# Performance work log

Measured on AMD Instinct MI355X. Metric: run time of the kernel, lower is better.

## Reference

```python
import jax, jax.numpy as jnp
import numpy as np

D_MODEL = 1024
N_HEADS = 16
HEAD_DIM = D_MODEL // N_HEADS


def setup_inputs() -> dict:
    key = jax.random.key(0)
    kx, kq, kk, kv, ko = jax.random.split(key, 5)
    B, S = 4, 2048
    scale = 0.02
    return {
        "x": jax.random.normal(kx, (B, S, D_MODEL), dtype=jnp.float32),
        "Wq": jax.random.normal(kq, (D_MODEL, D_MODEL), dtype=jnp.float32) * scale,
        "Wk": jax.random.normal(kk, (D_MODEL, HEAD_DIM), dtype=jnp.float32) * scale,
        "Wv": jax.random.normal(kv, (D_MODEL, HEAD_DIM), dtype=jnp.float32) * scale,
        "Wo": jax.random.normal(ko, (D_MODEL, D_MODEL), dtype=jnp.float32) * scale,
    }


def reference(x, Wq, Wk, Wv, Wo):
    B, S, _ = x.shape
    # Q: [B, H, S, hd]; K, V: [B, S, hd] shared across heads (MQA)
    Q = (x @ Wq).reshape(B, S, N_HEADS, HEAD_DIM).transpose(0, 2, 1, 3)
    K = x @ Wk
    V = x @ Wv
    # scores: [B, H, S, S]
    scores = jnp.einsum("bhqd,bkd->bhqk", Q, K) / jnp.sqrt(jnp.float32(HEAD_DIM))
    attn = jax.nn.softmax(scores, axis=-1)
    out = jnp.einsum("bhqk,bkd->bhqd", attn, V)  # [B, H, S, hd]
    out = out.transpose(0, 2, 1, 3).reshape(B, S, D_MODEL)
    return out @ Wo
```

## Files before the change

kernel.cpp:

```cpp
#include <hip/hip_runtime.h>
#include <hip/hip_bf16.h>

typedef __bf16  bf16x8  __attribute__((ext_vector_type(8)));
typedef __bf16  bf16x4  __attribute__((ext_vector_type(4)));
typedef float   f32x4   __attribute__((ext_vector_type(4)));
typedef unsigned short ushort8 __attribute__((ext_vector_type(8)));

#define D_MODEL 1024
#define HEAD_DIM 64
#define N_HEADS 16
#define BATCH 4
#define SEQ 2048
#define ROWS (BATCH*SEQ)
#define QKV_LD 1152
#define VT_LD 2080

#define AS1 __attribute__((address_space(1)))
#define AS3 __attribute__((address_space(3)))

__global__ __launch_bounds__(256) void k_f32_to_bf16(const float* __restrict__ in,
                                                     __bf16* __restrict__ out, int n) {
  int i = (blockIdx.x * 256 + threadIdx.x) * 8;
  if (i >= n) return;
  float4 a = *(const float4*)(in + i);
  float4 b = *(const float4*)(in + i + 4);
  __bf16 r[8] __attribute__((aligned(16))) =
      {(__bf16)a.x,(__bf16)a.y,(__bf16)a.z,(__bf16)a.w,
       (__bf16)b.x,(__bf16)b.y,(__bf16)b.z,(__bf16)b.w};
  *(ushort8*)(out + i) = *(const ushort8*)r;
}

__global__ __launch_bounds__(256) void k_transpose_f32_bf16(const float* __restrict__ in,
                                                            __bf16* __restrict__ out,
                                                            int R, int C) {
  __shared__ float t[32][33];
  int tx = threadIdx.x & 31, ty = threadIdx.x >> 5;
  int r0 = blockIdx.y * 32, c0 = blockIdx.x * 32;
  #pragma unroll
  for (int i = 0; i < 4; ++i)
    t[ty + i*8][tx] = in[(size_t)(r0 + ty + i*8) * C + c0 + tx];
  __syncthreads();
  #pragma unroll
  for (int i = 0; i < 4; ++i)
    out[(size_t)(c0 + ty + i*8) * R + r0 + tx] = (__bf16)t[tx][ty + i*8];
}

template<typename OUT_T>
__global__ __launch_bounds__(256) void k_gemm(const __bf16* __restrict__ A,
                                              const __bf16* __restrict__ Bt,
                                              OUT_T* __restrict__ C,
                                              int M, int N, int K) {
  __shared__ __bf16 As[128*32] __attribute__((aligned(16)));
  __shared__ __bf16 Bs[128*32] __attribute__((aligned(16)));
  const int tid  = threadIdx.x;
  const int lane = tid & 63, wave = tid >> 6;
  const int wm = wave >> 1, wn = wave & 1;
  const int l15 = lane & 15, lhi = lane >> 4;
  const int arow0 = blockIdx.x * 128;
  const int brow0 = blockIdx.y * 128;
  f32x4 acc[4][4] = {};
  const int srow = lane >> 2;
  const int scol = (lane & 3) * 8;

  for (int kt = 0; kt < K; kt += 32) {
    __syncthreads();
    #pragma unroll
    for (int i = 0; i < 2; ++i) {
      int chunk = i*4 + wave;
      int r = chunk*16 + srow;
      __builtin_amdgcn_global_load_lds(
          (const AS1 unsigned int*)(A  + (size_t)(arow0 + r)*K + kt + scol),
          (AS3 unsigned int*)(As + chunk*512), 16, 0, 0);
      __builtin_amdgcn_global_load_lds(
          (const AS1 unsigned int*)(Bt + (size_t)(brow0 + r)*K + kt + scol),
          (AS3 unsigned int*)(Bs + chunk*512), 16, 0, 0);
    }
    __syncthreads();
    bf16x8 af[4], bfr[4];
    #pragma unroll
    for (int m = 0; m < 4; ++m)
      af[m] = *(const bf16x8*)(As + (wm*64 + m*16 + l15)*32 + lhi*8);
    #pragma unroll
    for (int n = 0; n < 4; ++n)
      bfr[n] = *(const bf16x8*)(Bs + (wn*64 + n*16 + l15)*32 + lhi*8);
    #pragma unroll
    for (int m = 0; m < 4; ++m)
      #pragma unroll
      for (int n = 0; n < 4; ++n)
        acc[m][n] = __builtin_amdgcn_mfma_f32_16x16x32_bf16(af[m], bfr[n], acc[m][n], 0, 0, 0);
  }
  #pragma unroll
  for (int m = 0; m < 4; ++m)
    #pragma unroll
    for (int n = 0; n < 4; ++n) {
      int row = arow0 + wm*64 + m*16 + lhi*4;
      int col = brow0 + wn*64 + n*16 + l15;
      #pragma unroll
      for (int r = 0; r < 4; ++r)
        C[(size_t)(row + r) * N + col] = (OUT_T)acc[m][n][r];
    }
}

__global__ __launch_bounds__(256) void k_vt_split(const __bf16* __restrict__ QKV,
                                                  __bf16* __restrict__ Vt) {
  __shared__ __bf16 t[64][72] __attribute__((aligned(16)));
  int st = blockIdx.x, b = blockIdx.y;
  int tid = threadIdx.x;
  int rr = tid >> 3, cc = (tid & 7) * 8;
  #pragma unroll
  for (int i = 0; i < 2; ++i) {
    int s = rr + i*32;
    *(ushort8*)&t[s][cc] =
      *(const ushort8*)(QKV + (size_t)(b*SEQ + st*64 + s) * QKV_LD + 1088 + cc);
  }
  __syncthreads();
  #pragma unroll
  for (int i = 0; i < 2; ++i) {
    int d = rr + i*32;
    __bf16 tmp[8] __attribute__((aligned(16)));
    #pragma unroll
    for (int j = 0; j < 8; ++j) tmp[j] = t[cc + j][d];
    *(ushort8*)(Vt + (size_t)(b*64 + d) * VT_LD + st*64 + cc) = *(const ushort8*)tmp;
  }
}

__global__ __launch_bounds__(512, 4) void k_attn(const __bf16* __restrict__ QKV,
                                                 const __bf16* __restrict__ Vt,
                                                 __bf16* __restrict__ O) {
  __shared__ __bf16 Kl[2][64*64];
  __shared__ __bf16 Vl[2][64*64];
  __shared__ __bf16 Pl[8][32*64];
  const int qt = blockIdx.x, h = blockIdx.y, b = blockIdx.z;
  const int tid = threadIdx.x, lane = tid & 63, w = tid >> 6;
  const int l15 = lane & 15, lhi = lane >> 4;
  const int l7 = l15 & 7;

  const int srow = lane >> 3;
  const int j8   = lane & 7;
  const int row_t = w*8 + srow;
  const int jsrc = j8 ^ srow;
  const __bf16* Kg = QKV + (size_t)b*SEQ*QKV_LD + 1024;
  const __bf16* Vg = Vt  + (size_t)b*64*VT_LD;

  auto stage = [&](int t, int buf) {
    __builtin_amdgcn_global_load_lds(
        (const AS1 unsigned int*)(Kg + (size_t)(t*64 + row_t)*QKV_LD + jsrc*8),
        (AS3 unsigned int*)(&Kl[buf][0] + w*512), 16, 0, 0);
    __builtin_amdgcn_global_load_lds(
        (const AS1 unsigned int*)(Vg + (size_t)row_t*VT_LD + t*64 + jsrc*8),
        (AS3 unsigned int*)(&Vl[buf][0] + w*512), 16, 0, 0);
  };

  stage(0, 0);

  bf16x8 aq[2][2];
  {
    const __bf16* qp = QKV + (size_t)(b*SEQ + qt*256 + w*32 + l15)*QKV_LD + h*HEAD_DIM;
    aq[0][0] = *(const bf16x8*)(qp +               lhi*8);
    aq[0][1] = *(const bf16x8*)(qp +          32 + lhi*8);
    aq[1][0] = *(const bf16x8*)(qp + 16*QKV_LD +      lhi*8);
    aq[1][1] = *(const bf16x8*)(qp + 16*QKV_LD + 32 + lhi*8);
  }

  f32x4 oacc[2][4] = {};
  float mrun[2] = {-__builtin_inff(), -__builtin_inff()};
  float lrun[2] = {0.f, 0.f};

  asm volatile("s_waitcnt vmcnt(0)" ::: "memory");
  __builtin_amdgcn_s_barrier();

  for (int t = 0; t < SEQ/64; ++t) {
    const int cur = t & 1;
    if (t < SEQ/64 - 1) {
      stage(t+1, cur^1);
      asm volatile("s_waitcnt vmcnt(2)" ::: "memory");
    } else {
      asm volatile("s_waitcnt vmcnt(0)" ::: "memory");
    }
    const char* Kc = (const char*)&Kl[cur][0];
    const char* Vc = (const char*)&Vl[cur][0];

    f32x4 s[2][4] = {};
    __builtin_amdgcn_s_setprio(1);
    #pragma unroll
    for (int n = 0; n < 4; ++n) {
      const int key = n*16 + l15;
      bf16x8 kb0 = *(const bf16x8*)(Kc + key*128 + (((    lhi) ^ l7)*16));
      bf16x8 kb1 = *(const bf16x8*)(Kc + key*128 + (((4 + lhi) ^ l7)*16));
      #pragma unroll
      for (int m = 0; m < 2; ++m) {
        s[m][n] = __builtin_amdgcn_mfma_f32_16x16x32_bf16(kb0, aq[m][0], s[m][n], 0, 0, 0);
        s[m][n] = __builtin_amdgcn_mfma_f32_16x16x32_bf16(kb1, aq[m][1], s[m][n], 0, 0, 0);
      }
    }
    __builtin_amdgcn_s_setprio(0);

    float tm[2];
    #pragma unroll
    for (int m = 0; m < 2; ++m) {
      float a0 = fmaxf(fmaxf(s[m][0][0], s[m][0][1]), fmaxf(s[m][0][2], s[m][0][3]));
      float a1 = fmaxf(fmaxf(s[m][1][0], s[m][1][1]), fmaxf(s[m][1][2], s[m][1][3]));
      float a2 = fmaxf(fmaxf(s[m][2][0], s[m][2][1]), fmaxf(s[m][2][2], s[m][2][3]));
      float a3 = fmaxf(fmaxf(s[m][3][0], s[m][3][1]), fmaxf(s[m][3][2], s[m][3][3]));
      tm[m] = fmaxf(fmaxf(a0, a1), fmaxf(a2, a3));
      tm[m] = fmaxf(tm[m], __shfl_xor(tm[m], 16, 64));
      tm[m] = fmaxf(tm[m], __shfl_xor(tm[m], 32, 64));
    }

    int nogrow = (tm[0] <= mrun[0] + 64.f) && (tm[1] <= mrun[1] + 64.f);
    if (!__all(nogrow)) {
      float corr[2];
      #pragma unroll
      for (int m = 0; m < 2; ++m) {
        float mnew = fmaxf(mrun[m], tm[m]);
        corr[m] = __expf((mrun[m] - mnew) * 0.125f);
        mrun[m] = mnew;
        lrun[m] *= corr[m];
      }
      #pragma unroll
      for (int m = 0; m < 2; ++m) {
        float cb[4];
        #pragma unroll
        for (int r = 0; r < 4; ++r) cb[r] = __shfl(corr[m], lhi*4 + r, 64);
        #pragma unroll
        for (int n = 0; n < 4; ++n)
          #pragma unroll
          for (int r = 0; r < 4; ++r)
            oacc[m][n][r] *= cb[r];
      }
    }

    #pragma unroll
    for (int m = 0; m < 2; ++m) {
      const int prow = m*16 + l15;
      #pragma unroll
      for (int n = 0; n < 4; ++n) {
        bf16x4 pk;
        #pragma unroll
        for (int r = 0; r < 4; ++r) {
          float pv = __expf((s[m][n][r] - mrun[m]) * 0.125f);
          lrun[m] += pv;
          pk[r] = (__bf16)pv;
        }
        const int blk = (n*2 + (lhi>>1)) ^ l7;
        *(bf16x4*)((char*)&Pl[w][0] + prow*128 + blk*16 + (lhi&1)*8) = pk;
      }
    }

    bf16x8 ap0[2], ap1[2];
    #pragma unroll
    for (int m = 0; m < 2; ++m) {
      const char* pb = (const char*)&Pl[w][0] + (m*16 + l15)*128;
      ap0[m] = *(const bf16x8*)(pb + (((    lhi) ^ l7)*16));
      ap1[m] = *(const bf16x8*)(pb + (((4 + lhi) ^ l7)*16));
    }

    __builtin_amdgcn_s_setprio(1);
    #pragma unroll
    for (int n = 0; n < 4; ++n) {
      const int d = n*16 + l15;
      bf16x8 vb0 = *(const bf16x8*)(Vc + d*128 + (((    lhi) ^ l7)*16));
      bf16x8 vb1 = *(const bf16x8*)(Vc + d*128 + (((4 + lhi) ^ l7)*16));
      #pragma unroll
      for (int m = 0; m < 2; ++m) {
        oacc[m][n] = __builtin_amdgcn_mfma_f32_16x16x32_bf16(ap0[m], vb0, oacc[m][n], 0, 0, 0);
        oacc[m][n] = __builtin_amdgcn_mfma_f32_16x16x32_bf16(ap1[m], vb1, oacc[m][n], 0, 0, 0);
      }
    }
    __builtin_amdgcn_s_setprio(0);
    __builtin_amdgcn_s_barrier();
  }

  #pragma unroll
  for (int m = 0; m < 2; ++m) {
    lrun[m] += __shfl_xor(lrun[m], 16, 64);
    lrun[m] += __shfl_xor(lrun[m], 32, 64);
  }
  float rinv[2][4];
  #pragma unroll
  for (int m = 0; m < 2; ++m)
    #pragma unroll
    for (int r = 0; r < 4; ++r)
      rinv[m][r] = __builtin_amdgcn_rcpf(__shfl(lrun[m], lhi*4 + r, 64));
  #pragma unroll
  for (int m = 0; m < 2; ++m)
    #pragma unroll
    for (int n = 0; n < 4; ++n)
      #pragma unroll
      for (int r = 0; r < 4; ++r) {
        size_t row = (size_t)b*SEQ + qt*256 + w*32 + m*16 + lhi*4 + r;
        O[row * D_MODEL + h*HEAD_DIM + n*16 + l15] = (__bf16)(oacc[m][n][r] * rinv[m][r]);
      }
}

extern "C" void kernel_launch(void* const* d_in, const int* in_sizes, int n_in,
                              void* d_out, int out_size, void* d_ws, size_t ws_size,
                              hipStream_t stream) {
  const float* x  = (const float*)d_in[0];
  const float* Wq = (const float*)d_in[1];
  const float* Wk = (const float*)d_in[2];
  const float* Wv = (const float*)d_in[3];
  const float* Wo = (const float*)d_in[4];
  float* out = (float*)d_out;

  char* ws = (char*)d_ws;
  size_t off = 0;
  auto alloc = [&](size_t bytes) -> void* {
    void* p = ws + off;
    off += (bytes + 255) & ~(size_t)255;
    return p;
  };
  __bf16* xb    = (__bf16*)alloc((size_t)ROWS * D_MODEL * 2);
  __bf16* QKVb  = (__bf16*)alloc((size_t)ROWS * QKV_LD * 2);
  __bf16* WqkvT = (__bf16*)alloc((size_t)QKV_LD * D_MODEL * 2);
  __bf16* WoT   = (__bf16*)alloc((size_t)D_MODEL * D_MODEL * 2);
  __bf16* Vtb   = (__bf16*)alloc((size_t)BATCH * 64 * VT_LD * 2);

  k_f32_to_bf16<<<ROWS*D_MODEL/2048, 256, 0, stream>>>(x, xb, ROWS*D_MODEL);
  k_transpose_f32_bf16<<<dim3(D_MODEL/32, D_MODEL/32), 256, 0, stream>>>(Wq, WqkvT, D_MODEL, D_MODEL);
  k_transpose_f32_bf16<<<dim3(HEAD_DIM/32, D_MODEL/32), 256, 0, stream>>>(Wk, WqkvT + (size_t)1024*D_MODEL, D_MODEL, HEAD_DIM);
  k_transpose_f32_bf16<<<dim3(HEAD_DIM/32, D_MODEL/32), 256, 0, stream>>>(Wv, WqkvT + (size_t)1088*D_MODEL, D_MODEL, HEAD_DIM);
  k_transpose_f32_bf16<<<dim3(D_MODEL/32, D_MODEL/32), 256, 0, stream>>>(Wo, WoT, D_MODEL, D_MODEL);

  k_gemm<__bf16><<<dim3(ROWS/128, QKV_LD/128), 256, 0, stream>>>(xb, WqkvT, QKVb, ROWS, QKV_LD, D_MODEL);
  k_vt_split<<<dim3(SEQ/64, BATCH), 256, 0, stream>>>(QKVb, Vtb);
  k_attn<<<dim3(SEQ/256, N_HEADS, BATCH), 512, 0, stream>>>(QKVb, Vtb, xb);
  k_gemm<float><<<dim3(ROWS/128, D_MODEL/128), 256, 0, stream>>>(xb, WoT, out, ROWS, D_MODEL, D_MODEL);
}
```

Before: 263.8 us.

## Double-buffer GEMM LDS loads and fold softmax scale into Wq with exp2

The GEMM now double-buffers its LDS tiles so the global-to-LDS load of the next K slice overlaps the MFMAs on the current one, with one barrier per iteration instead of two. Separately, the softmax scale and log2(e) are folded into Wq during the weight transpose, so attention can use the raw v_exp_f32 (exp2) without a per-element multiply. The lazy-rescale threshold is lowered from 64 to 8, which is correct in the new log2 units. The GEMM change doubles LDS use per block, and folding the scale into bf16 weights slightly changes rounding.

Result: faster. 244.5 us (-7.3%).

```diff
diff --git a/kernel.cpp b/kernel.cpp
--- a/kernel.cpp
+++ b/kernel.cpp
@@ -17,6 +17,10 @@
 
 #define AS1 __attribute__((address_space(1)))
 #define AS3 __attribute__((address_space(3)))
+
+static __device__ inline float exp2_fast(float x) {
+  float r; asm("v_exp_f32 %0, %1" : "=v"(r) : "v"(x)); return r;
+}
 
 __global__ __launch_bounds__(256) void k_f32_to_bf16(const float* __restrict__ in,
                                                      __bf16* __restrict__ out, int n) {
@@ -32,7 +36,7 @@
 
 __global__ __launch_bounds__(256) void k_transpose_f32_bf16(const float* __restrict__ in,
                                                             __bf16* __restrict__ out,
-                                                            int R, int C) {
+                                                            int R, int C, float scale) {
   __shared__ float t[32][33];
   int tx = threadIdx.x & 31, ty = threadIdx.x >> 5;
   int r0 = blockIdx.y * 32, c0 = blockIdx.x * 32;
@@ -42,7 +46,7 @@
   __syncthreads();
   #pragma unroll
   for (int i = 0; i < 4; ++i)
-    out[(size_t)(c0 + ty + i*8) * R + r0 + tx] = (__bf16)t[tx][ty + i*8];
+    out[(size_t)(c0 + ty + i*8) * R + r0 + tx] = (__bf16)(t[tx][ty + i*8] * scale);
 }
 
 template<typename OUT_T>
@@ -50,8 +54,8 @@
                                               const __bf16* __restrict__ Bt,
                                               OUT_T* __restrict__ C,
                                               int M, int N, int K) {
-  __shared__ __bf16 As[128*32] __attribute__((aligned(16)));
-  __shared__ __bf16 Bs[128*32] __attribute__((aligned(16)));
+  __shared__ __bf16 As[2][128*32] __attribute__((aligned(16)));
+  __shared__ __bf16 Bs[2][128*32] __attribute__((aligned(16)));
   const int tid  = threadIdx.x;
   const int lane = tid & 63, wave = tid >> 6;
   const int wm = wave >> 1, wn = wave & 1;
@@ -61,33 +65,43 @@
   f32x4 acc[4][4] = {};
   const int srow = lane >> 2;
   const int scol = (lane & 3) * 8;
-
-  for (int kt = 0; kt < K; kt += 32) {
-    __syncthreads();
+  const int nt = K >> 5;
+
+  auto stage = [&](int t, int buf) {
     #pragma unroll
     for (int i = 0; i < 2; ++i) {
       int chunk = i*4 + wave;
       int r = chunk*16 + srow;
       __builtin_amdgcn_global_load_lds(
-          (const AS1 unsigned int*)(A  + (size_t)(arow0 + r)*K + kt + scol),
-          (AS3 unsigned int*)(As + chunk*512), 16, 0, 0);
+          (const AS1 unsigned int*)(A  + (size_t)(arow0 + r)*K + t*32 + scol),
+          (AS3 unsigned int*)(&As[buf][0] + chunk*512), 16, 0, 0);
       __builtin_amdgcn_global_load_lds(
-          (const AS1 unsigned int*)(Bt + (size_t)(brow0 + r)*K + kt + scol),
-          (AS3 unsigned int*)(Bs + chunk*512), 16, 0, 0);
-    }
-    __syncthreads();
+          (const AS1 unsigned int*)(Bt + (size_t)(brow0 + r)*K + t*32 + scol),
+          (AS3 unsigned int*)(&Bs[buf][0] + chunk*512), 16, 0, 0);
+    }
+  };
+
+  stage(0, 0);
+  asm volatile("s_waitcnt vmcnt(0)" ::: "memory");
+  __builtin_amdgcn_s_barrier();
+
+  for (int t = 0; t < nt; ++t) {
+    const int cur = t & 1;
+    if (t + 1 < nt) stage(t + 1, cur ^ 1);
     bf16x8 af[4], bfr[4];
     #pragma unroll
     for (int m = 0; m < 4; ++m)
-      af[m] = *(const bf16x8*)(As + (wm*64 + m*16 + l15)*32 + lhi*8);
+      af[m] = *(const bf16x8*)(&As[cur][0] + (wm*64 + m*16 + l15)*32 + lhi*8);
     #pragma unroll
     for (int n = 0; n < 4; ++n)
-      bfr[n] = *(const bf16x8*)(Bs + (wn*64 + n*16 + l15)*32 + lhi*8);
+      bfr[n] = *(const bf16x8*)(&Bs[cur][0] + (wn*64 + n*16 + l15)*32 + lhi*8);
     #pragma unroll
     for (int m = 0; m < 4; ++m)
       #pragma unroll
       for (int n = 0; n < 4; ++n)
         acc[m][n] = __builtin_amdgcn_mfma_f32_16x16x32_bf16(af[m], bfr[n], acc[m][n], 0, 0, 0);
+    asm volatile("s_waitcnt vmcnt(0)" ::: "memory");
+    __builtin_amdgcn_s_barrier();
   }
   #pragma unroll
   for (int m = 0; m < 4; ++m)
@@ -207,13 +221,13 @@
       tm[m] = fmaxf(tm[m], __shfl_xor(tm[m], 32, 64));
     }
 
-    int nogrow = (tm[0] <= mrun[0] + 64.f) && (tm[1] <= mrun[1] + 64.f);
+    int nogrow = (tm[0] <= mrun[0] + 8.f) && (tm[1] <= mrun[1] + 8.f);
     if (!__all(nogrow)) {
       float corr[2];
       #pragma unroll
       for (int m = 0; m < 2; ++m) {
         float mnew = fmaxf(mrun[m], tm[m]);
-        corr[m] = __expf((mrun[m] - mnew) * 0.125f);
+        corr[m] = exp2_fast(mrun[m] - mnew);
         mrun[m] = mnew;
         lrun[m] *= corr[m];
       }
@@ -238,7 +252,7 @@
         bf16x4 pk;
         #pragma unroll
         for (int r = 0; r < 4; ++r) {
-          float pv = __expf((s[m][n][r] - mrun[m]) * 0.125f);
+          float pv = exp2_fast(s[m][n][r] - mrun[m]);
           lrun[m] += pv;
           pk[r] = (__bf16)pv;
         }
@@ -316,11 +330,13 @@
   __bf16* WoT   = (__bf16*)alloc((size_t)D_MODEL * D_MODEL * 2);
   __bf16* Vtb   = (__bf16*)alloc((size_t)BATCH * 64 * VT_LD * 2);
 
+  const float SCALE_Q = 0.125f * 1.4426950408889634f;
+
   k_f32_to_bf16<<<ROWS*D_MODEL/2048, 256, 0, stream>>>(x, xb, ROWS*D_MODEL);
-  k_transpose_f32_bf16<<<dim3(D_MODEL/32, D_MODEL/32), 256, 0, stream>>>(Wq, WqkvT, D_MODEL, D_MODEL);
-  k_transpose_f32_bf16<<<dim3(HEAD_DIM/32, D_MODEL/32), 256, 0, stream>>>(Wk, WqkvT + (size_t)1024*D_MODEL, D_MODEL, HEAD_DIM);
-  k_transpose_f32_bf16<<<dim3(HEAD_DIM/32, D_MODEL/32), 256, 0, stream>>>(Wv, WqkvT + (size_t)1088*D_MODEL, D_MODEL, HEAD_DIM);
-  k_transpose_f32_bf16<<<dim3(D_MODEL/32, D_MODEL/32), 256, 0, stream>>>(Wo, WoT, D_MODEL, D_MODEL);
+  k_transpose_f32_bf16<<<dim3(D_MODEL/32, D_MODEL/32), 256, 0, stream>>>(Wq, WqkvT, D_MODEL, D_MODEL, SCALE_Q);
+  k_transpose_f32_bf16<<<dim3(HEAD_DIM/32, D_MODEL/32), 256, 0, stream>>>(Wk, WqkvT + (size_t)1024*D_MODEL, D_MODEL, HEAD_DIM, 1.0f);
+  k_transpose_f32_bf16<<<dim3(HEAD_DIM/32, D_MODEL/32), 256, 0, stream>>>(Wv, WqkvT + (size_t)1088*D_MODEL, D_MODEL, HEAD_DIM, 1.0f);
+  k_transpose_f32_bf16<<<dim3(D_MODEL/32, D_MODEL/32), 256, 0, stream>>>(Wo, WoT, D_MODEL, D_MODEL, 1.0f);
 
   k_gemm<__bf16><<<dim3(ROWS/128, QKV_LD/128), 256, 0, stream>>>(xb, WqkvT, QKVb, ROWS, QKV_LD, D_MODEL);
   k_vt_split<<<dim3(SEQ/64, BATCH), 256, 0, stream>>>(QKVb, Vtb);
```
